# Optimization experiments

Measured on AMD Instinct MI355X. Metric: run time of the kernel, lower is better.

## Reference

```python
import jax, jax.numpy as jnp
import numpy as np
from jax import lax


def _l2norm(x):
    # normalize rows: x / ||x||_2, matching torch vector_norm along dim=-1
    return x / jnp.linalg.norm(x, axis=-1, keepdims=True)


def setup_inputs() -> dict:
    key = jax.random.key(0)
    k1, k2, k3, k4, k5 = jax.random.split(key, 5)
    B, N, Ds, Dd = 64, 20000, 4096, 2048
    return {
        "f_content": jax.random.normal(k1, (B, Ds), dtype=jnp.float32),
        "f_distorsion": jax.random.normal(k2, (B, Dd), dtype=jnp.float32),
        "semantic_db": jax.random.normal(k3, (N, Ds), dtype=jnp.float32),
        "distorsion_db": jax.random.normal(k4, (N, Dd), dtype=jnp.float32),
        "metrics": jax.random.uniform(k5, (N,), dtype=jnp.float32),
        "K": 9,
    }


def reference(f_content, f_distorsion, semantic_db, distorsion_db, metrics, K):
    # L2-normalize query features and DB features (DB is normalized at init in torch)
    fc = _l2norm(f_content)            # [B, Ds]
    fd = _l2norm(f_distorsion)         # [B, Dd]
    sem_db = _l2norm(semantic_db)      # [N, Ds]
    dst_db = _l2norm(distorsion_db)    # [N, Dd]

    # full cosine similarity matmuls, then descending top-K (== sort desc + slice K)
    sem_cos = fc @ sem_db.T            # [B, N]
    dst_cos = fd @ dst_db.T            # [B, N]
    _, idx_sem = lax.top_k(sem_cos, K)   # [B, K]
    _, idx_dst = lax.top_k(dst_cos, K)   # [B, K]

    # gather metric values for retrieved neighbors; interleave sem/dst per m
    m_sem = metrics[idx_sem]           # [B, K]
    m_dst = metrics[idx_dst]           # [B, K]
    retrieved = jnp.stack([m_sem, m_dst], axis=-1).reshape(m_sem.shape[0], 2 * K)  # [B, 2K]
    result = retrieved.mean(axis=-1)   # [B]
    return result, retrieved
```

## Files before the change

kernel.cpp:

```cpp
#include <hip/hip_runtime.h>
#include <math.h>


typedef _Float16 half8 __attribute__((ext_vector_type(8)));
typedef float    f32x4 __attribute__((ext_vector_type(4)));

#define NDB   20000
#define NQ    64
#define KSEM  4096
#define KDST  2048
#define KC    2048
#define NSTEP (KC / 64)
#define BN    64
#define NTILE 313

__device__ __forceinline__ void async_cp16(const void* g, void* l) {
    __builtin_amdgcn_global_load_lds(
        (const __attribute__((address_space(1))) void*)g,
        (__attribute__((address_space(3))) void*)l, 16, 0, 0);
}

__global__ __launch_bounds__(256) void qsplit_kernel(
    const float* __restrict__ fc, const float* __restrict__ fd,
    _Float16* __restrict__ apack_sem, _Float16* __restrict__ apack_dst)
{
    const int idx = (int)blockIdx.x * 256 + (int)threadIdx.x;
    const int NSEM8 = NQ * KSEM / 8;
    const float* src; _Float16* dst; int row, g8, K;
    if (idx < NSEM8) { src = fc; dst = apack_sem; K = KSEM; row = idx >> 9; g8 = idx & 511; }
    else { const int j = idx - NSEM8; src = fd; dst = apack_dst; K = KDST; row = j >> 8; g8 = j & 255; }

    const float* p = src + (size_t)row * K + g8 * 8;
    const float4 v0 = ((const float4*)p)[0];
    const float4 v1 = ((const float4*)p)[1];
    const float xs[8] = {v0.x, v0.y, v0.z, v0.w, v1.x, v1.y, v1.z, v1.w};
    half8 hi, lo;
    #pragma unroll
    for (int e = 0; e < 8; ++e) {
        const _Float16 h = (_Float16)xs[e];
        hi[e] = h;
        lo[e] = (_Float16)((xs[e] - (float)h) * 4096.0f);
    }
    const int sec = g8 >> 2, kg = g8 & 3;
    const int u = (row << 2) + (((row >> 1) & 3) ^ kg);
    half8* d8 = (half8*)dst;
    d8[sec * 512 + u]       = hi;
    d8[sec * 512 + 256 + u] = lo;
}

__global__ __launch_bounds__(256, 2) void score_kernel(
    const float* __restrict__ sdb, const float* __restrict__ ddb,
    const _Float16* __restrict__ apack_sem, const _Float16* __restrict__ apack_dst,
    float* __restrict__ semp0, float* __restrict__ semp1, float* __restrict__ dstp,
    float* __restrict__ nsq0, float* __restrict__ nsq1, float* __restrict__ nsqd)
{
    __shared__ __align__(16) _Float16 A_lds[2][8192];
    __shared__ __align__(16) float    B_lds[2][4096];

    const int tid  = threadIdx.x;
    const int lane = tid & 63, w = tid >> 6;
    const int bid  = (int)blockIdx.x;
    const int mkc  = bid / NTILE;
    const int nt   = bid % NTILE;
    const int n0   = nt * BN;

    const float* D; const _Float16* AP; float *SOUT, *NOUT; int Ks, koff;
    if (mkc == 0)      { D=sdb; AP=apack_sem; SOUT=semp0; NOUT=nsq0; Ks=KSEM; koff=0;  }
    else if (mkc == 1) { D=sdb; AP=apack_sem; SOUT=semp1; NOUT=nsq1; Ks=KSEM; koff=KC; }
    else               { D=ddb; AP=apack_dst; SOUT=dstp;  NOUT=nsqd; Ks=KDST; koff=0;  }

    const int u0 = w * 128 + lane,      r0 = u0 >> 3, c0 = (u0 & 7) ^ (r0 & 7);
    const int u1 = u0 + 64,             r1 = u1 >> 3, c1 = (u1 & 7) ^ (r1 & 7);
    const int rg0 = (n0 + r0 < NDB) ? n0 + r0 : NDB - 1;
    const int rg1 = (n0 + r1 < NDB) ? n0 + r1 : NDB - 1;
    const float* gB0 = D + (size_t)rg0 * Ks + koff + c0 * 4;
    const float* gB1 = D + (size_t)rg1 * Ks + koff + c1 * 4;
    const uint4* gA = (const uint4*)AP + ((size_t)koff >> 5) * 512 + w * 64 + lane;

    const int lr = lane & 15, kg = lane >> 4;
    const int qh = w >> 1, nh = w & 1;
    const int rowA0 = qh * 32 + lr;
    const int rowA1 = rowA0 + 16;
    const int uA0 = ((rowA0 << 2) + (((rowA0 >> 1) & 3) ^ kg)) * 8;
    const int uA1 = ((rowA1 << 2) + (((rowA1 >> 1) & 3) ^ kg)) * 8;
    const int rB0 = nh * 32 + lr;
    const int rB1 = rB0 + 16;
    const int oB00 = rB0 * 32 + (((kg * 2 + 0) ^ (rB0 & 7)) << 2);
    const int oB01 = rB0 * 32 + (((kg * 2 + 1) ^ (rB0 & 7)) << 2);
    const int oB10 = rB1 * 32 + (((kg * 2 + 0) ^ (rB1 & 7)) << 2);
    const int oB11 = rB1 * 32 + (((kg * 2 + 1) ^ (rB1 & 7)) << 2);

    f32x4 acc_h[2][2], acc_x[2][2];
    const f32x4 zz = {0.f, 0.f, 0.f, 0.f};
    #pragma unroll
    for (int i = 0; i < 2; ++i)
        #pragma unroll
        for (int j = 0; j < 2; ++j) { acc_h[i][j] = zz; acc_x[i][j] = zz; }
    float sq0 = 0.f, sq1 = 0.f;

    auto STAGE = [&](int s, int buf) {
        #pragma unroll
        for (int sec = 0; sec < 2; ++sec) {
            const size_t gsec = (size_t)(2 * s + sec);
            async_cp16(gA + gsec * 512,       &A_lds[buf][sec * 4096 + w * 512]);
            async_cp16(gA + gsec * 512 + 256, &A_lds[buf][sec * 4096 + 2048 + w * 512]);
            async_cp16(gB0 + gsec * 32, &B_lds[buf][sec * 2048 + w * 512]);
            async_cp16(gB1 + gsec * 32, &B_lds[buf][sec * 2048 + w * 512 + 256]);
        }
    };

    auto COMPUTE = [&](int buf) {
        #pragma unroll
        for (int sec = 0; sec < 2; ++sec) {
            const float*    Bb = &B_lds[buf][sec * 2048];
            const _Float16* Ab = &A_lds[buf][sec * 4096];
            half8 bh0, bl0, bh1, bl1;
            {
                const f32x4 p = *(const f32x4*)(Bb + oB00);
                const f32x4 q = *(const f32x4*)(Bb + oB01);
                const float xs[8] = {p[0], p[1], p[2], p[3], q[0], q[1], q[2], q[3]};
                #pragma unroll
                for (int e = 0; e < 8; ++e) {
                    const float x = xs[e];
                    sq0 = fmaf(x, x, sq0);
                    const _Float16 h = (_Float16)x;
                    bh0[e] = h;
                    bl0[e] = (_Float16)((x - (float)h) * 4096.0f);
                }
            }
            {
                const f32x4 p = *(const f32x4*)(Bb + oB10);
                const f32x4 q = *(const f32x4*)(Bb + oB11);
                const float xs[8] = {p[0], p[1], p[2], p[3], q[0], q[1], q[2], q[3]};
                #pragma unroll
                for (int e = 0; e < 8; ++e) {
                    const float x = xs[e];
                    sq1 = fmaf(x, x, sq1);
                    const _Float16 h = (_Float16)x;
                    bh1[e] = h;
                    bl1[e] = (_Float16)((x - (float)h) * 4096.0f);
                }
            }
            const half8 ah0 = *(const half8*)(Ab + uA0);
            const half8 av0 = *(const half8*)(Ab + 2048 + uA0);
            const half8 ah1 = *(const half8*)(Ab + uA1);
            const half8 av1 = *(const half8*)(Ab + 2048 + uA1);

            acc_h[0][0] = __builtin_amdgcn_mfma_f32_16x16x32_f16(ah0, bh0, acc_h[0][0], 0, 0, 0);
            acc_x[0][0] = __builtin_amdgcn_mfma_f32_16x16x32_f16(ah0, bl0, acc_x[0][0], 0, 0, 0);
            acc_x[0][0] = __builtin_amdgcn_mfma_f32_16x16x32_f16(av0, bh0, acc_x[0][0], 0, 0, 0);
            acc_h[0][1] = __builtin_amdgcn_mfma_f32_16x16x32_f16(ah0, bh1, acc_h[0][1], 0, 0, 0);
            acc_x[0][1] = __builtin_amdgcn_mfma_f32_16x16x32_f16(ah0, bl1, acc_x[0][1], 0, 0, 0);
            acc_x[0][1] = __builtin_amdgcn_mfma_f32_16x16x32_f16(av0, bh1, acc_x[0][1], 0, 0, 0);
            acc_h[1][0] = __builtin_amdgcn_mfma_f32_16x16x32_f16(ah1, bh0, acc_h[1][0], 0, 0, 0);
            acc_x[1][0] = __builtin_amdgcn_mfma_f32_16x16x32_f16(ah1, bl0, acc_x[1][0], 0, 0, 0);
            acc_x[1][0] = __builtin_amdgcn_mfma_f32_16x16x32_f16(av1, bh0, acc_x[1][0], 0, 0, 0);
            acc_h[1][1] = __builtin_amdgcn_mfma_f32_16x16x32_f16(ah1, bh1, acc_h[1][1], 0, 0, 0);
            acc_x[1][1] = __builtin_amdgcn_mfma_f32_16x16x32_f16(ah1, bl1, acc_x[1][1], 0, 0, 0);
            acc_x[1][1] = __builtin_amdgcn_mfma_f32_16x16x32_f16(av1, bh1, acc_x[1][1], 0, 0, 0);
        }
    };

    STAGE(0, 0); STAGE(1, 1);

    for (int s = 0; s < NSTEP; ++s) {
        if (s < NSTEP - 1) { asm volatile("s_waitcnt vmcnt(8)" ::: "memory"); }
        else               { asm volatile("s_waitcnt vmcnt(0)" ::: "memory"); }
        __builtin_amdgcn_s_barrier();
        COMPUTE(s & 1);
        __builtin_amdgcn_s_barrier();
        if (s + 2 < NSTEP) STAGE(s + 2, s & 1);
    }

    sq0 += __shfl_xor(sq0, 16); sq0 += __shfl_xor(sq0, 32);
    sq1 += __shfl_xor(sq1, 16); sq1 += __shfl_xor(sq1, 32);
    if (qh == 0 && lane < 16) {
        const int nn0 = n0 + nh * 32 + lane;
        const int nn1 = nn0 + 16;
        if (nn0 < NDB) NOUT[nn0] = sq0;
        if (nn1 < NDB) NOUT[nn1] = sq1;
    }

    #pragma unroll
    for (int i = 0; i < 2; ++i)
        #pragma unroll
        for (int j = 0; j < 2; ++j) {
            const int n = n0 + nh * 32 + j * 16 + lr;
            if (n < NDB) {
                #pragma unroll
                for (int rr = 0; rr < 4; ++rr) {
                    const int q = qh * 32 + i * 16 + kg * 4 + rr;
                    SOUT[(size_t)q * NDB + n] = acc_h[i][j][rr] + acc_x[i][j][rr] * (1.0f / 4096.0f);
                }
            }
        }
}

__global__ __launch_bounds__(256) void topk_kernel(
    const float* __restrict__ semp0, const float* __restrict__ semp1,
    const float* __restrict__ dstp,
    const float* __restrict__ nsq0, const float* __restrict__ nsq1,
    const float* __restrict__ nsqd,
    const float* __restrict__ metrics, float* __restrict__ out_ret)
{
    __shared__ float sv[256][9];
    __shared__ int   si[256][9];

    const int tid = threadIdx.x;
    const int b = (int)blockIdx.x & 63;
    const int m = (int)blockIdx.x >> 6;

    float v[9]; int ix[9];
    #pragma unroll
    for (int k = 0; k < 9; ++k) { v[k] = -INFINITY; ix[k] = 0x7fffffff; }

    const size_t roff = (size_t)b * NDB;
    for (int i = tid; i < NDB; i += 256) {
        float sval;
        if (m == 0) {
            const float s = semp0[roff + i] + semp1[roff + i];
            sval = s * (1.0f / sqrtf(nsq0[i] + nsq1[i]));
        } else {
            sval = dstp[roff + i] * (1.0f / sqrtf(nsqd[i]));
        }
        if (sval > v[0]) {
            bool bt[9];
            bt[0] = true;
            #pragma unroll
            for (int j = 1; j < 9; ++j) bt[j] = sval > v[j];
            #pragma unroll
            for (int j = 0; j < 8; ++j) {
                v[j]  = bt[j+1] ? v[j+1]  : (bt[j] ? sval : v[j]);
                ix[j] = bt[j+1] ? ix[j+1] : (bt[j] ? i    : ix[j]);
            }
            v[8]  = bt[8] ? sval : v[8];
            ix[8] = bt[8] ? i    : ix[8];
        }
    }

    #pragma unroll
    for (int k = 0; k < 9; ++k) { sv[tid][k] = v[k]; si[tid][k] = ix[k]; }
    __syncthreads();

    for (int s2 = 128; s2 >= 1; s2 >>= 1) {
        if (tid < s2) {
            float rv[9]; int ri[9];
            int pa = 8, pb = 8;
            #pragma unroll
            for (int k = 8; k >= 0; --k) {
                const float va = sv[tid][pa];      const int ia = si[tid][pa];
                const float vb = sv[tid + s2][pb]; const int ib = si[tid + s2][pb];
                const bool takeA = (va > vb) || (va == vb && ia < ib);
                rv[k] = takeA ? va : vb;
                ri[k] = takeA ? ia : ib;
                if (takeA) --pa; else --pb;
            }
            #pragma unroll
            for (int k = 0; k < 9; ++k) { sv[tid][k] = rv[k]; si[tid][k] = ri[k]; }
        }
        __syncthreads();
    }

    if (tid < 9) {
        const int idx = si[0][8 - tid];
        out_ret[(size_t)b * 18 + 2 * tid + m] = metrics[idx];
    }
}

__global__ void finalize_kernel(float* __restrict__ d_out)
{
    const int b = threadIdx.x;
    const float* r = d_out + 64 + (size_t)b * 18;
    float s = 0.f;
    #pragma unroll
    for (int j = 0; j < 18; ++j) s += r[j];
    d_out[b] = s * (1.0f / 18.0f);
}

extern "C" void kernel_launch(void* const* d_in, const int* in_sizes, int n_in,
                              void* d_out, int out_size, void* d_ws, size_t ws_size,
                              hipStream_t stream)
{
    const float* fc  = (const float*)d_in[0];
    const float* fd  = (const float*)d_in[1];
    const float* sdb = (const float*)d_in[2];
    const float* ddb = (const float*)d_in[3];
    const float* met = (const float*)d_in[4];

    float* semp0 = (float*)d_ws;
    float* semp1 = semp0 + (size_t)NQ * NDB;
    float* dstp  = semp1 + (size_t)NQ * NDB;
    float* nsq0  = dstp  + (size_t)NQ * NDB;
    float* nsq1  = nsq0 + NDB;
    float* nsqd  = nsq1 + NDB;
    _Float16* apack_sem = (_Float16*)(nsqd + NDB);
    _Float16* apack_dst = apack_sem + (size_t)NQ * KSEM * 2;

    float* out = (float*)d_out;

    qsplit_kernel<<<dim3(192), dim3(256), 0, stream>>>(fc, fd, apack_sem, apack_dst);
    score_kernel<<<dim3(3 * NTILE), dim3(256), 0, stream>>>(
        sdb, ddb, apack_sem, apack_dst, semp0, semp1, dstp, nsq0, nsq1, nsqd);
    topk_kernel<<<dim3(128), dim3(256), 0, stream>>>(
        semp0, semp1, dstp, nsq0, nsq1, nsqd, met, out + 64);
    finalize_kernel<<<dim3(1), dim3(64), 0, stream>>>(out);
}
```

Measured before the change: 183.0 us.

## Use single fp16 MFMA scoring with top-16 candidates and exact fp32 rerank

Drops the hi/lo fp16 split emulation of fp32 in the score GEMM and uses one fp16 MFMA per tile, cutting the matrix work by about three times and halving the packed query storage. To recover accuracy, the top-k pass keeps 16 candidates per query instead of 9. A new rerank kernel recomputes exact fp32 cosines for those candidates and picks the final 9. The score kernel also moves to 512-thread blocks with 128-row DB tiles. The risk is that a true top-9 neighbor falls outside the fp16 top-16 and is lost.

After: 217.6 us. 1.19x slower.

```diff
diff --git a/kernel.cpp b/kernel.cpp
--- a/kernel.cpp
+++ b/kernel.cpp
@@ -5,14 +5,15 @@
 typedef _Float16 half8 __attribute__((ext_vector_type(8)));
 typedef float    f32x4 __attribute__((ext_vector_type(4)));
 
-#define NDB   20000
-#define NQ    64
-#define KSEM  4096
-#define KDST  2048
-#define KC    2048
-#define NSTEP (KC / 64)
-#define BN    64
-#define NTILE 313
+#define NDB    20000
+#define NQ     64
+#define KSEM   4096
+#define KDST   2048
+#define KC     2048
+#define NSTEP  (KC / 64)
+#define BN2    128
+#define NTILE2 157
+#define K2     16
 
 __device__ __forceinline__ void async_cp16(const void* g, void* l) {
     __builtin_amdgcn_global_load_lds(
@@ -34,98 +35,96 @@
     const float4 v0 = ((const float4*)p)[0];
     const float4 v1 = ((const float4*)p)[1];
     const float xs[8] = {v0.x, v0.y, v0.z, v0.w, v1.x, v1.y, v1.z, v1.w};
-    half8 hi, lo;
-    #pragma unroll
-    for (int e = 0; e < 8; ++e) {
-        const _Float16 h = (_Float16)xs[e];
-        hi[e] = h;
-        lo[e] = (_Float16)((xs[e] - (float)h) * 4096.0f);
-    }
+    half8 hi;
+    #pragma unroll
+    for (int e = 0; e < 8; ++e) hi[e] = (_Float16)xs[e];
     const int sec = g8 >> 2, kg = g8 & 3;
     const int u = (row << 2) + (((row >> 1) & 3) ^ kg);
-    half8* d8 = (half8*)dst;
-    d8[sec * 512 + u]       = hi;
-    d8[sec * 512 + 256 + u] = lo;
-}
-
-__global__ __launch_bounds__(256, 2) void score_kernel(
+    ((half8*)dst)[sec * 256 + u] = hi;
+}
+
+__global__ __launch_bounds__(512, 4) void score_kernel(
     const float* __restrict__ sdb, const float* __restrict__ ddb,
     const _Float16* __restrict__ apack_sem, const _Float16* __restrict__ apack_dst,
     float* __restrict__ semp0, float* __restrict__ semp1, float* __restrict__ dstp,
     float* __restrict__ nsq0, float* __restrict__ nsq1, float* __restrict__ nsqd)
 {
-    __shared__ __align__(16) _Float16 A_lds[2][8192];
-    __shared__ __align__(16) float    B_lds[2][4096];
+    __shared__ __align__(16) _Float16 A_lds[2][4096];
+    __shared__ __align__(16) float    B_lds[2][8192];
 
     const int tid  = threadIdx.x;
     const int lane = tid & 63, w = tid >> 6;
     const int bid  = (int)blockIdx.x;
-    const int mkc  = bid / NTILE;
-    const int nt   = bid % NTILE;
-    const int n0   = nt * BN;
+    const int mkc  = bid / NTILE2;
+    const int nt   = bid % NTILE2;
+    const int n0   = nt * BN2;
 
     const float* D; const _Float16* AP; float *SOUT, *NOUT; int Ks, koff;
     if (mkc == 0)      { D=sdb; AP=apack_sem; SOUT=semp0; NOUT=nsq0; Ks=KSEM; koff=0;  }
     else if (mkc == 1) { D=sdb; AP=apack_sem; SOUT=semp1; NOUT=nsq1; Ks=KSEM; koff=KC; }
     else               { D=ddb; AP=apack_dst; SOUT=dstp;  NOUT=nsqd; Ks=KDST; koff=0;  }
 
-    const int u0 = w * 128 + lane,      r0 = u0 >> 3, c0 = (u0 & 7) ^ (r0 & 7);
-    const int u1 = u0 + 64,             r1 = u1 >> 3, c1 = (u1 & 7) ^ (r1 & 7);
-    const int rg0 = (n0 + r0 < NDB) ? n0 + r0 : NDB - 1;
-    const int rg1 = (n0 + r1 < NDB) ? n0 + r1 : NDB - 1;
-    const float* gB0 = D + (size_t)rg0 * Ks + koff + c0 * 4;
-    const float* gB1 = D + (size_t)rg1 * Ks + koff + c1 * 4;
-    const uint4* gA = (const uint4*)AP + ((size_t)koff >> 5) * 512 + w * 64 + lane;
+    int   rB[2], rgB[2];
+    const float* bbase[2];
+    #pragma unroll
+    for (int q = 0; q < 2; ++q) {
+        const int u = w * 128 + q * 64 + lane;
+        const int r = u >> 3;
+        const int csrc = (u & 7) ^ (r & 7);
+        rB[q] = r;
+        rgB[q] = (n0 + r < NDB) ? n0 + r : NDB - 1;
+        bbase[q] = D + (size_t)rgB[q] * Ks + koff + csrc * 4;
+    }
+    const int secA = w >> 2;
+    const uint4* abase = (const uint4*)AP + ((size_t)koff >> 5) * 256
+                         + (size_t)secA * 256 + (w & 3) * 64 + lane;
 
     const int lr = lane & 15, kg = lane >> 4;
-    const int qh = w >> 1, nh = w & 1;
-    const int rowA0 = qh * 32 + lr;
-    const int rowA1 = rowA0 + 16;
+    const int qh = w >> 2, nh = w & 3;
+    const int rowA0 = qh * 32 + lr, rowA1 = rowA0 + 16;
     const int uA0 = ((rowA0 << 2) + (((rowA0 >> 1) & 3) ^ kg)) * 8;
     const int uA1 = ((rowA1 << 2) + (((rowA1 >> 1) & 3) ^ kg)) * 8;
-    const int rB0 = nh * 32 + lr;
-    const int rB1 = rB0 + 16;
-    const int oB00 = rB0 * 32 + (((kg * 2 + 0) ^ (rB0 & 7)) << 2);
-    const int oB01 = rB0 * 32 + (((kg * 2 + 1) ^ (rB0 & 7)) << 2);
-    const int oB10 = rB1 * 32 + (((kg * 2 + 0) ^ (rB1 & 7)) << 2);
-    const int oB11 = rB1 * 32 + (((kg * 2 + 1) ^ (rB1 & 7)) << 2);
-
-    f32x4 acc_h[2][2], acc_x[2][2];
+    const int rF0 = nh * 32 + lr, rF1 = rF0 + 16;
+    const int oB00 = rF0 * 32 + (((kg * 2 + 0) ^ (rF0 & 7)) << 2);
+    const int oB01 = rF0 * 32 + (((kg * 2 + 1) ^ (rF0 & 7)) << 2);
+    const int oB10 = rF1 * 32 + (((kg * 2 + 0) ^ (rF1 & 7)) << 2);
+    const int oB11 = rF1 * 32 + (((kg * 2 + 1) ^ (rF1 & 7)) << 2);
+
+    f32x4 acc[2][2];
     const f32x4 zz = {0.f, 0.f, 0.f, 0.f};
     #pragma unroll
     for (int i = 0; i < 2; ++i)
         #pragma unroll
-        for (int j = 0; j < 2; ++j) { acc_h[i][j] = zz; acc_x[i][j] = zz; }
+        for (int j = 0; j < 2; ++j) acc[i][j] = zz;
     float sq0 = 0.f, sq1 = 0.f;
 
     auto STAGE = [&](int s, int buf) {
+        async_cp16(abase + (size_t)s * 512, &A_lds[buf][secA * 2048 + (w & 3) * 512]);
         #pragma unroll
         for (int sec = 0; sec < 2; ++sec) {
-            const size_t gsec = (size_t)(2 * s + sec);
-            async_cp16(gA + gsec * 512,       &A_lds[buf][sec * 4096 + w * 512]);
-            async_cp16(gA + gsec * 512 + 256, &A_lds[buf][sec * 4096 + 2048 + w * 512]);
-            async_cp16(gB0 + gsec * 32, &B_lds[buf][sec * 2048 + w * 512]);
-            async_cp16(gB1 + gsec * 32, &B_lds[buf][sec * 2048 + w * 512 + 256]);
+            const int kofs = (2 * s + sec) * 32;
+            #pragma unroll
+            for (int q = 0; q < 2; ++q) {
+                async_cp16(bbase[q] + kofs,
+                           &B_lds[buf][sec * 4096 + (w * 128 + q * 64) * 4]);
+            }
         }
     };
 
     auto COMPUTE = [&](int buf) {
         #pragma unroll
         for (int sec = 0; sec < 2; ++sec) {
-            const float*    Bb = &B_lds[buf][sec * 2048];
-            const _Float16* Ab = &A_lds[buf][sec * 4096];
-            half8 bh0, bl0, bh1, bl1;
+            const float*    Bb = &B_lds[buf][sec * 4096];
+            const _Float16* Ab = &A_lds[buf][sec * 2048];
+            half8 bh0, bh1;
             {
                 const f32x4 p = *(const f32x4*)(Bb + oB00);
                 const f32x4 q = *(const f32x4*)(Bb + oB01);
                 const float xs[8] = {p[0], p[1], p[2], p[3], q[0], q[1], q[2], q[3]};
                 #pragma unroll
                 for (int e = 0; e < 8; ++e) {
-                    const float x = xs[e];
-                    sq0 = fmaf(x, x, sq0);
-                    const _Float16 h = (_Float16)x;
-                    bh0[e] = h;
-                    bl0[e] = (_Float16)((x - (float)h) * 4096.0f);
+                    sq0 = fmaf(xs[e], xs[e], sq0);
+                    bh0[e] = (_Float16)xs[e];
                 }
             }
             {
@@ -134,37 +133,23 @@
                 const float xs[8] = {p[0], p[1], p[2], p[3], q[0], q[1], q[2], q[3]};
                 #pragma unroll
                 for (int e = 0; e < 8; ++e) {
-                    const float x = xs[e];
-                    sq1 = fmaf(x, x, sq1);
-                    const _Float16 h = (_Float16)x;
-                    bh1[e] = h;
-                    bl1[e] = (_Float16)((x - (float)h) * 4096.0f);
+                    sq1 = fmaf(xs[e], xs[e], sq1);
+                    bh1[e] = (_Float16)xs[e];
                 }
             }
             const half8 ah0 = *(const half8*)(Ab + uA0);
-            const half8 av0 = *(const half8*)(Ab + 2048 + uA0);
             const half8 ah1 = *(const half8*)(Ab + uA1);
-            const half8 av1 = *(const half8*)(Ab + 2048 + uA1);
-
-            acc_h[0][0] = __builtin_amdgcn_mfma_f32_16x16x32_f16(ah0, bh0, acc_h[0][0], 0, 0, 0);
-            acc_x[0][0] = __builtin_amdgcn_mfma_f32_16x16x32_f16(ah0, bl0, acc_x[0][0], 0, 0, 0);
-            acc_x[0][0] = __builtin_amdgcn_mfma_f32_16x16x32_f16(av0, bh0, acc_x[0][0], 0, 0, 0);
-            acc_h[0][1] = __builtin_amdgcn_mfma_f32_16x16x32_f16(ah0, bh1, acc_h[0][1], 0, 0, 0);
-            acc_x[0][1] = __builtin_amdgcn_mfma_f32_16x16x32_f16(ah0, bl1, acc_x[0][1], 0, 0, 0);
-            acc_x[0][1] = __builtin_amdgcn_mfma_f32_16x16x32_f16(av0, bh1, acc_x[0][1], 0, 0, 0);
-            acc_h[1][0] = __builtin_amdgcn_mfma_f32_16x16x32_f16(ah1, bh0, acc_h[1][0], 0, 0, 0);
-            acc_x[1][0] = __builtin_amdgcn_mfma_f32_16x16x32_f16(ah1, bl0, acc_x[1][0], 0, 0, 0);
-            acc_x[1][0] = __builtin_amdgcn_mfma_f32_16x16x32_f16(av1, bh0, acc_x[1][0], 0, 0, 0);
-            acc_h[1][1] = __builtin_amdgcn_mfma_f32_16x16x32_f16(ah1, bh1, acc_h[1][1], 0, 0, 0);
-            acc_x[1][1] = __builtin_amdgcn_mfma_f32_16x16x32_f16(ah1, bl1, acc_x[1][1], 0, 0, 0);
-            acc_x[1][1] = __builtin_amdgcn_mfma_f32_16x16x32_f16(av1, bh1, acc_x[1][1], 0, 0, 0);
+            acc[0][0] = __builtin_amdgcn_mfma_f32_16x16x32_f16(ah0, bh0, acc[0][0], 0, 0, 0);
+            acc[0][1] = __builtin_amdgcn_mfma_f32_16x16x32_f16(ah0, bh1, acc[0][1], 0, 0, 0);
+            acc[1][0] = __builtin_amdgcn_mfma_f32_16x16x32_f16(ah1, bh0, acc[1][0], 0, 0, 0);
+            acc[1][1] = __builtin_amdgcn_mfma_f32_16x16x32_f16(ah1, bh1, acc[1][1], 0, 0, 0);
         }
     };
 
     STAGE(0, 0); STAGE(1, 1);
 
     for (int s = 0; s < NSTEP; ++s) {
-        if (s < NSTEP - 1) { asm volatile("s_waitcnt vmcnt(8)" ::: "memory"); }
+        if (s < NSTEP - 1) { asm volatile("s_waitcnt vmcnt(5)" ::: "memory"); }
         else               { asm volatile("s_waitcnt vmcnt(0)" ::: "memory"); }
         __builtin_amdgcn_s_barrier();
         COMPUTE(s & 1);
@@ -190,7 +175,7 @@
                 #pragma unroll
                 for (int rr = 0; rr < 4; ++rr) {
                     const int q = qh * 32 + i * 16 + kg * 4 + rr;
-                    SOUT[(size_t)q * NDB + n] = acc_h[i][j][rr] + acc_x[i][j][rr] * (1.0f / 4096.0f);
+                    SOUT[(size_t)q * NDB + n] = acc[i][j][rr];
                 }
             }
         }
@@ -201,53 +186,52 @@
     const float* __restrict__ dstp,
     const float* __restrict__ nsq0, const float* __restrict__ nsq1,
     const float* __restrict__ nsqd,
-    const float* __restrict__ metrics, float* __restrict__ out_ret)
-{
-    __shared__ float sv[256][9];
-    __shared__ int   si[256][9];
+    int* __restrict__ idx_ws)
+{
+    __shared__ float sv[256][K2];
+    __shared__ int   si[256][K2];
 
     const int tid = threadIdx.x;
     const int b = (int)blockIdx.x & 63;
     const int m = (int)blockIdx.x >> 6;
 
-    float v[9]; int ix[9];
-    #pragma unroll
-    for (int k = 0; k < 9; ++k) { v[k] = -INFINITY; ix[k] = 0x7fffffff; }
+    float v[K2]; int ix[K2];
+    #pragma unroll
+    for (int k = 0; k < K2; ++k) { v[k] = -INFINITY; ix[k] = 0x7fffffff; }
 
     const size_t roff = (size_t)b * NDB;
     for (int i = tid; i < NDB; i += 256) {
         float sval;
         if (m == 0) {
-            const float s = semp0[roff + i] + semp1[roff + i];
-            sval = s * (1.0f / sqrtf(nsq0[i] + nsq1[i]));
+            sval = (semp0[roff + i] + semp1[roff + i]) * (1.0f / sqrtf(nsq0[i] + nsq1[i]));
         } else {
             sval = dstp[roff + i] * (1.0f / sqrtf(nsqd[i]));
         }
         if (sval > v[0]) {
-            bool bt[9];
+            bool bt[K2];
             bt[0] = true;
             #pragma unroll
-            for (int j = 1; j < 9; ++j) bt[j] = sval > v[j];
-            #pragma unroll
-            for (int j = 0; j < 8; ++j) {
+            for (int j = 1; j < K2; ++j) bt[j] = sval > v[j];
+            #pragma unroll
+            for (int j = 0; j < K2 - 1; ++j) {
                 v[j]  = bt[j+1] ? v[j+1]  : (bt[j] ? sval : v[j]);
                 ix[j] = bt[j+1] ? ix[j+1] : (bt[j] ? i    : ix[j]);
             }
-            v[8]  = bt[8] ? sval : v[8];
-            ix[8] = bt[8] ? i    : ix[8];
-        }
-    }
-
-    #pragma unroll
-    for (int k = 0; k < 9; ++k) { sv[tid][k] = v[k]; si[tid][k] = ix[k]; }
+            v[K2-1]  = bt[K2-1] ? sval : v[K2-1];
+            ix[K2-1] = bt[K2-1] ? i    : ix[K2-1];
+        }
+    }
+
+    #pragma unroll
+    for (int k = 0; k < K2; ++k) { sv[tid][k] = v[k]; si[tid][k] = ix[k]; }
     __syncthreads();
 
     for (int s2 = 128; s2 >= 1; s2 >>= 1) {
         if (tid < s2) {
-            float rv[9]; int ri[9];
-            int pa = 8, pb = 8;
-            #pragma unroll
-            for (int k = 8; k >= 0; --k) {
+            float rv[K2]; int ri[K2];
+            int pa = K2 - 1, pb = K2 - 1;
+            #pragma unroll
+            for (int k = K2 - 1; k >= 0; --k) {
                 const float va = sv[tid][pa];      const int ia = si[tid][pa];
                 const float vb = sv[tid + s2][pb]; const int ib = si[tid + s2][pb];
                 const bool takeA = (va > vb) || (va == vb && ia < ib);
@@ -256,14 +240,67 @@
                 if (takeA) --pa; else --pb;
             }
             #pragma unroll
-            for (int k = 0; k < 9; ++k) { sv[tid][k] = rv[k]; si[tid][k] = ri[k]; }
+            for (int k = 0; k < K2; ++k) { sv[tid][k] = rv[k]; si[tid][k] = ri[k]; }
         }
         __syncthreads();
     }
 
-    if (tid < 9) {
-        const int idx = si[0][8 - tid];
-        out_ret[(size_t)b * 18 + 2 * tid + m] = metrics[idx];
+    if (tid < K2) idx_ws[(size_t)blockIdx.x * K2 + tid] = si[0][K2 - 1 - tid];
+}
+
+__global__ __launch_bounds__(256) void rerank_kernel(
+    const float* __restrict__ fc, const float* __restrict__ fd,
+    const float* __restrict__ sdb, const float* __restrict__ ddb,
+    const int* __restrict__ idx_ws, const float* __restrict__ metrics,
+    float* __restrict__ out_ret)
+{
+    __shared__ float cosv[K2];
+    __shared__ int   cidx[K2];
+
+    const int tid = threadIdx.x;
+    const int lane = tid & 63, w = tid >> 6;
+    const int bid = (int)blockIdx.x;
+    const int b = bid & 63;
+    const int m = bid >> 6;
+
+    const float* Q  = (m == 0) ? fc + (size_t)b * KSEM : fd + (size_t)b * KDST;
+    const float* DB = (m == 0) ? sdb : ddb;
+    const int Ks = (m == 0) ? KSEM : KDST;
+    const int nf4 = Ks / 4;
+
+    for (int c = w; c < K2; c += 4) {
+        const int idx = idx_ws[(size_t)bid * K2 + c];
+        const float4* Q4 = (const float4*)Q;
+        const float4* R4 = (const float4*)(DB + (size_t)idx * Ks);
+        float dot = 0.f, sq = 0.f;
+        for (int it = lane; it < nf4; it += 64) {
+            const float4 qv = Q4[it];
+            const float4 rv = R4[it];
+            dot = fmaf(qv.x, rv.x, dot); sq = fmaf(rv.x, rv.x, sq);
+            dot = fmaf(qv.y, rv.y, dot); sq = fmaf(rv.y, rv.y, sq);
+            dot = fmaf(qv.z, rv.z, dot); sq = fmaf(rv.z, rv.z, sq);
+            dot = fmaf(qv.w, rv.w, dot); sq = fmaf(rv.w, rv.w, sq);
+        }
+        #pragma unroll
+        for (int off = 1; off < 64; off <<= 1) {
+            dot += __shfl_xor(dot, off);
+            sq  += __shfl_xor(sq,  off);
+        }
+        if (lane == 0) {
+            cosv[c] = dot / sqrtf(sq);
+            cidx[c] = idx;
+        }
+    }
+    __syncthreads();
+
+    if (tid < K2) {
+        const float v = cosv[tid];
+        const int   id = cidx[tid];
+        int rank = 0;
+        #pragma unroll
+        for (int j = 0; j < K2; ++j)
+            rank += (cosv[j] > v) || (cosv[j] == v && cidx[j] < id);
+        if (rank < 9) out_ret[(size_t)b * 18 + 2 * rank + m] = metrics[id];
     }
 }
 
@@ -294,14 +331,17 @@
     float* nsq1  = nsq0 + NDB;
     float* nsqd  = nsq1 + NDB;
     _Float16* apack_sem = (_Float16*)(nsqd + NDB);
-    _Float16* apack_dst = apack_sem + (size_t)NQ * KSEM * 2;
+    _Float16* apack_dst = apack_sem + (size_t)NQ * KSEM;
+    int* idx_ws = (int*)(apack_dst + (size_t)NQ * KDST);
 
     float* out = (float*)d_out;
 
     qsplit_kernel<<<dim3(192), dim3(256), 0, stream>>>(fc, fd, apack_sem, apack_dst);
-    score_kernel<<<dim3(3 * NTILE), dim3(256), 0, stream>>>(
+    score_kernel<<<dim3(3 * NTILE2), dim3(512), 0, stream>>>(
         sdb, ddb, apack_sem, apack_dst, semp0, semp1, dstp, nsq0, nsq1, nsqd);
     topk_kernel<<<dim3(128), dim3(256), 0, stream>>>(
-        semp0, semp1, dstp, nsq0, nsq1, nsqd, met, out + 64);
+        semp0, semp1, dstp, nsq0, nsq1, nsqd, idx_ws);
+    rerank_kernel<<<dim3(128), dim3(256), 0, stream>>>(
+        fc, fd, sdb, ddb, idx_ws, met, out + 64);
     finalize_kernel<<<dim3(1), dim3(64), 0, stream>>>(out);
 }
```

## Split top-k over 8 row segments per query and add merge kernel

Applied to the files above, without the earlier changes.

The single-block-per-(query,modality) top-k is split into 8 segment blocks per row. Each segment keeps 16 candidates, and a new merge kernel picks the global top-9 by rank counting and gathers the metrics. This targets the low occupancy of the old top-k pass, which ran only 128 blocks on a large GPU. In exchange it adds an extra launch and a wider per-thread register top-list.

After: 169.6 us. -7.4%, faster.

```diff
diff --git a/kernel.cpp b/kernel.cpp
--- a/kernel.cpp
+++ b/kernel.cpp
@@ -13,6 +13,9 @@
 #define NSTEP (KC / 64)
 #define BN    64
 #define NTILE 313
+#define K2    16
+#define SEG   8
+#define SEGSZ (NDB / SEG)
 
 __device__ __forceinline__ void async_cp16(const void* g, void* l) {
     __builtin_amdgcn_global_load_lds(
@@ -196,58 +199,60 @@
         }
 }
 
-__global__ __launch_bounds__(256) void topk_kernel(
+__global__ __launch_bounds__(256) void topk_seg_kernel(
     const float* __restrict__ semp0, const float* __restrict__ semp1,
     const float* __restrict__ dstp,
     const float* __restrict__ nsq0, const float* __restrict__ nsq1,
     const float* __restrict__ nsqd,
-    const float* __restrict__ metrics, float* __restrict__ out_ret)
-{
-    __shared__ float sv[256][9];
-    __shared__ int   si[256][9];
+    float* __restrict__ cand_val, int* __restrict__ cand_idx)
+{
+    __shared__ float sv[256][K2];
+    __shared__ int   si[256][K2];
 
     const int tid = threadIdx.x;
-    const int b = (int)blockIdx.x & 63;
-    const int m = (int)blockIdx.x >> 6;
-
-    float v[9]; int ix[9];
-    #pragma unroll
-    for (int k = 0; k < 9; ++k) { v[k] = -INFINITY; ix[k] = 0x7fffffff; }
+    const int mb  = (int)blockIdx.x >> 3;
+    const int seg = (int)blockIdx.x & 7;
+    const int b = mb & 63;
+    const int m = mb >> 6;
+
+    float v[K2]; int ix[K2];
+    #pragma unroll
+    for (int k = 0; k < K2; ++k) { v[k] = -INFINITY; ix[k] = 0x7fffffff; }
 
     const size_t roff = (size_t)b * NDB;
-    for (int i = tid; i < NDB; i += 256) {
+    const int iend = (seg + 1) * SEGSZ;
+    for (int i = seg * SEGSZ + tid; i < iend; i += 256) {
         float sval;
         if (m == 0) {
-            const float s = semp0[roff + i] + semp1[roff + i];
-            sval = s * (1.0f / sqrtf(nsq0[i] + nsq1[i]));
+            sval = (semp0[roff + i] + semp1[roff + i]) * (1.0f / sqrtf(nsq0[i] + nsq1[i]));
         } else {
             sval = dstp[roff + i] * (1.0f / sqrtf(nsqd[i]));
         }
         if (sval > v[0]) {
-            bool bt[9];
+            bool bt[K2];
             bt[0] = true;
             #pragma unroll
-            for (int j = 1; j < 9; ++j) bt[j] = sval > v[j];
+            for (int j = 1; j < K2; ++j) bt[j] = sval > v[j];
             #pragma unroll
-            for (int j = 0; j < 8; ++j) {
+            for (int j = 0; j < K2 - 1; ++j) {
                 v[j]  = bt[j+1] ? v[j+1]  : (bt[j] ? sval : v[j]);
                 ix[j] = bt[j+1] ? ix[j+1] : (bt[j] ? i    : ix[j]);
             }
-            v[8]  = bt[8] ? sval : v[8];
-            ix[8] = bt[8] ? i    : ix[8];
-        }
-    }
-
-    #pragma unroll
-    for (int k = 0; k < 9; ++k) { sv[tid][k] = v[k]; si[tid][k] = ix[k]; }
+            v[K2-1]  = bt[K2-1] ? sval : v[K2-1];
+            ix[K2-1] = bt[K2-1] ? i    : ix[K2-1];
+        }
+    }
+
+    #pragma unroll
+    for (int k = 0; k < K2; ++k) { sv[tid][k] = v[k]; si[tid][k] = ix[k]; }
     __syncthreads();
 
     for (int s2 = 128; s2 >= 1; s2 >>= 1) {
         if (tid < s2) {
-            float rv[9]; int ri[9];
-            int pa = 8, pb = 8;
+            float rv[K2]; int ri[K2];
+            int pa = K2 - 1, pb = K2 - 1;
             #pragma unroll
-            for (int k = 8; k >= 0; --k) {
+            for (int k = K2 - 1; k >= 0; --k) {
                 const float va = sv[tid][pa];      const int ia = si[tid][pa];
                 const float vb = sv[tid + s2][pb]; const int ib = si[tid + s2][pb];
                 const bool takeA = (va > vb) || (va == vb && ia < ib);
@@ -256,15 +261,36 @@
                 if (takeA) --pa; else --pb;
             }
             #pragma unroll
-            for (int k = 0; k < 9; ++k) { sv[tid][k] = rv[k]; si[tid][k] = ri[k]; }
+            for (int k = 0; k < K2; ++k) { sv[tid][k] = rv[k]; si[tid][k] = ri[k]; }
         }
         __syncthreads();
     }
 
-    if (tid < 9) {
-        const int idx = si[0][8 - tid];
-        out_ret[(size_t)b * 18 + 2 * tid + m] = metrics[idx];
-    }
+    if (tid < K2) {
+        cand_val[(size_t)mb * 128 + seg * K2 + tid] = sv[0][K2 - 1 - tid];
+        cand_idx[(size_t)mb * 128 + seg * K2 + tid] = si[0][K2 - 1 - tid];
+    }
+}
+
+__global__ __launch_bounds__(128) void merge_kernel(
+    const float* __restrict__ cand_val, const int* __restrict__ cand_idx,
+    const float* __restrict__ metrics, float* __restrict__ out_ret)
+{
+    __shared__ float v[128];
+    __shared__ int   id[128];
+    const int tid = threadIdx.x;
+    const int mb  = (int)blockIdx.x;
+    const int b = mb & 63;
+    const int m = mb >> 6;
+    v[tid]  = cand_val[(size_t)mb * 128 + tid];
+    id[tid] = cand_idx[(size_t)mb * 128 + tid];
+    __syncthreads();
+    const float mv = v[tid];
+    const int   mi = id[tid];
+    int rank = 0;
+    for (int j = 0; j < 128; ++j)
+        rank += (v[j] > mv) || (v[j] == mv && id[j] < mi);
+    if (rank < 9) out_ret[(size_t)b * 18 + 2 * rank + m] = metrics[mi];
 }
 
 __global__ void finalize_kernel(float* __restrict__ d_out)
@@ -295,13 +321,16 @@
     float* nsqd  = nsq1 + NDB;
     _Float16* apack_sem = (_Float16*)(nsqd + NDB);
     _Float16* apack_dst = apack_sem + (size_t)NQ * KSEM * 2;
+    float* cand_val = (float*)(apack_dst + (size_t)NQ * KDST * 2);
+    int*   cand_idx = (int*)(cand_val + 128 * 128);
 
     float* out = (float*)d_out;
 
     qsplit_kernel<<<dim3(192), dim3(256), 0, stream>>>(fc, fd, apack_sem, apack_dst);
     score_kernel<<<dim3(3 * NTILE), dim3(256), 0, stream>>>(
         sdb, ddb, apack_sem, apack_dst, semp0, semp1, dstp, nsq0, nsq1, nsqd);
-    topk_kernel<<<dim3(128), dim3(256), 0, stream>>>(
-        semp0, semp1, dstp, nsq0, nsq1, nsqd, met, out + 64);
+    topk_seg_kernel<<<dim3(128 * SEG), dim3(256), 0, stream>>>(
+        semp0, semp1, dstp, nsq0, nsq1, nsqd, cand_val, cand_idx);
+    merge_kernel<<<dim3(128), dim3(128), 0, stream>>>(cand_val, cand_idx, met, out + 64);
     finalize_kernel<<<dim3(1), dim3(64), 0, stream>>>(out);
 }
```
